# Kernel optimization log

Measured on AMD Instinct MI355X. Metric: run time of the kernel, lower is better.

Reference implementation:

```python
import jax, jax.numpy as jnp
import numpy as np

ALPHA = 1.0
MIN_FEATURE_SIZE = 1.0
SC = 1e-12
EPS_V_FLOOR = 1e-32 ** (1.0 / 6.0)  # ~4.64e-6, floor on gradient magnitude


def setup_inputs() -> dict:
    key = jax.random.key(0)
    eps = jax.random.normal(key, (8192, 8192), dtype=jnp.float32)
    grid_size = jnp.asarray(0.05, dtype=jnp.float32)
    return {"eps": eps, "grid_size": grid_size}


def _ls_derivatives(phi, d):
    # torch.gradient == numpy.gradient with edge_order=1 (central interior, one-sided edges)
    phi_x, phi_y = jnp.gradient(phi, d, d)
    phi_x = phi_x + SC
    phi_y = phi_y + SC
    phi_xx, phi_xy = jnp.gradient(phi_x, d, d)        # second derivs of phi_x
    phi_yy = jnp.gradient(phi_y, d, axis=1)           # only d/dy of phi_y is used
    return phi_x, phi_y, phi_xx, phi_xy, phi_yy


def reference(eps, grid_size):
    ex, ey, exx, exy, eyy = _ls_derivatives(eps, grid_size)
    pi_d = jnp.pi / (1.1 * MIN_FEATURE_SIZE)
    eps_v = jnp.maximum(jnp.sqrt(ex * ex + ey * ey), jnp.float32(EPS_V_FLOOR))
    k = (ex * ex * eyy - 2.0 * ex * ey * exy + ey * ey * exx) / (eps_v ** 3)
    curve_const = jnp.abs(k * jnp.arctan(eps_v / (eps + 1e-6))) - pi_d
    return jnp.nansum(ALPHA * jnp.maximum(curve_const, 0.0) * grid_size ** 2)
```

## Files before the change

kernel.cpp:

```cpp
#include <hip/hip_runtime.h>
#include <math.h>


typedef float f2 __attribute__((ext_vector_type(2)));
typedef float f4 __attribute__((ext_vector_type(4)));

constexpr float SCF = 1e-12f;
constexpr float EVF = 4.6415888336e-6f;
constexpr float PID = 2.8559933214452666f;
constexpr float PIH = 1.5707963268f;
constexpr int   RS  = 64;

struct Row { f4 lo, hi; };

__device__ __forceinline__ float C(const Row& r, int k) {
    return k < 4 ? r.lo[k] : r.hi[k - 4];
}
__device__ __forceinline__ void load_row(Row& r, const float* p) {
    r.lo = *(const f4*)p;
    r.hi = *(const f4*)(p + 4);
}
__device__ __forceinline__ f2 mk(float a, float b) { f2 v; v.x = a; v.y = b; return v; }
__device__ __forceinline__ f2 fma2(f2 a, f2 b, f2 c) { return __builtin_elementwise_fma(a, b, c); }
__device__ __forceinline__ f2 max2(f2 a, f2 b) { return __builtin_elementwise_max(a, b); }
__device__ __forceinline__ f2 min2(f2 a, f2 b) { return __builtin_elementwise_min(a, b); }
__device__ __forceinline__ f2 abs2(f2 a) { return __builtin_elementwise_abs(a); }
__device__ __forceinline__ f2 rcp2(f2 a) {
    return mk(__builtin_amdgcn_rcpf(a.x), __builtin_amdgcn_rcpf(a.y));
}
__device__ __forceinline__ f2 rsq2(f2 a) {
    return mk(__builtin_amdgcn_rsqf(a.x), __builtin_amdgcn_rsqf(a.y));
}

__device__ __forceinline__ f2 compute_pair(const Row& R0, const Row& R1,
                                           const Row& R2, const Row& R3,
                                           const Row& R4, const Row& R5,
                                           f2 c1, f2 c2) {
    f2 dif[6];
    #pragma unroll
    for (int k = 0; k < 6; ++k)
        dif[k] = mk(C(R3, k + 1) - C(R1, k + 1),
                    C(R4, k + 1) - C(R2, k + 1));
    f2 Pz[8];
    #pragma unroll
    for (int k = 0; k < 8; ++k)
        Pz[k] = mk(C(R2, k), C(R3, k));

    f2 part = mk(0.0f, 0.0f);
    #pragma unroll
    for (int q = 0; q < 4; ++q) {
        const f2 c00  = Pz[q + 2];
        const f2 u    = dif[q + 1];
        const f2 v    = Pz[q + 3] - Pz[q + 1];
        const f2 exxr = fma2(mk(-2.0f, -2.0f), c00,
                             mk(C(R4, q + 2) + C(R0, q + 2),
                                C(R5, q + 2) + C(R1, q + 2)));
        const f2 eyyr = fma2(mk(-2.0f, -2.0f), c00, Pz[q + 4] + Pz[q]);
        const f2 exyr = dif[q + 2] - dif[q];

        const f2 uu  = u * u;
        const f2 vv  = v * v;
        const f2 r2  = uu + vv;
        const f2 rsq = rsq2(r2);
        const f2 N   = fma2(uu, eyyr, fma2(-2.0f * (u * v), exyr, vv * exxr));
        const f2 r3  = rsq * rsq * rsq;
        const f2 kabs = abs2(N) * min2(c1 * r3, c2);
        const f2 ev   = max2(c1 * (r2 * rsq), mk(EVF, EVF));

        const f2 aw = abs2(c00 + 1e-6f);
        const f2 mx = max2(ev, aw);
        const f2 mn = min2(ev, aw);
        const f2 t  = mn * rcp2(mx);
        const f2 t2 = t * t;
        f2 pl = fma2(t2, mk(-0.01172120f, -0.01172120f), mk(0.05265332f, 0.05265332f));
        pl = fma2(t2, pl, mk(-0.11643287f, -0.11643287f));
        pl = fma2(t2, pl, mk(0.19354346f, 0.19354346f));
        pl = fma2(t2, pl, mk(-0.33262347f, -0.33262347f));
        pl = fma2(t2, pl, mk(0.99997726f, 0.99997726f));
        pl = pl * t;
        f2 at;
        at.x = (ev.x > aw.x) ? PIH - pl.x : pl.x;
        at.y = (ev.y > aw.y) ? PIH - pl.y : pl.y;

        part = part + max2(fma2(kabs, at, mk(-PID, -PID)), mk(0.0f, 0.0f));
    }
    return part;
}

__device__ __forceinline__ float eg(const float* __restrict__ e, int n, int i, int j) {
    return e[(size_t)i * (size_t)n + j];
}
__device__ __forceinline__ float gex(const float* __restrict__ e, int n, int i, int j,
                                     float inv_d, float inv_2d) {
    float v;
    if (i == 0)          v = (eg(e, n, 1, j) - eg(e, n, 0, j)) * inv_d;
    else if (i == n - 1) v = (eg(e, n, n - 1, j) - eg(e, n, n - 2, j)) * inv_d;
    else                 v = (eg(e, n, i + 1, j) - eg(e, n, i - 1, j)) * inv_2d;
    return v + SCF;
}
__device__ __forceinline__ float gey(const float* __restrict__ e, int n, int i, int j,
                                     float inv_d, float inv_2d) {
    float v;
    if (j == 0)          v = (eg(e, n, i, 1) - eg(e, n, i, 0)) * inv_d;
    else if (j == n - 1) v = (eg(e, n, i, n - 1) - eg(e, n, i, n - 2)) * inv_d;
    else                 v = (eg(e, n, i, j + 1) - eg(e, n, i, j - 1)) * inv_2d;
    return v + SCF;
}

__global__ __launch_bounds__(256, 4)
void fab_fused(const float* __restrict__ eps, const float* __restrict__ gs,
               float* __restrict__ ws, int n, int G2, int nfr) {
    const float d      = *gs;
    const float inv_2d = 0.5f / d;
    const float c1s    = inv_2d;
    const float c2s    = 1e16f * (inv_2d * inv_2d) * (inv_2d * inv_2d);

    float acc = 0.0f;

    const int gg = blockIdx.x * 256 + threadIdx.x;
    const bool valid = gg < G2;
    const int gc = min(gg, G2 - 1);
    const int i0 = 2 + RS * blockIdx.y;
    const int count = min(RS, (n - 2) - i0);
    const float*  pj = eps + 4 * (size_t)gc;
    const size_t  sn = (size_t)n;

    Row s0, s1, s2, s3, s4, s5, s6, s7;
    load_row(s0, pj + (size_t)(i0 - 2) * sn);
    load_row(s1, pj + (size_t)(i0 - 1) * sn);
    load_row(s2, pj + (size_t)(i0    ) * sn);
    load_row(s3, pj + (size_t)(i0 + 1) * sn);
    load_row(s4, pj + (size_t)(i0 + 2) * sn);
    load_row(s5, pj + (size_t)(i0 + 3) * sn);
    const float* pnext = pj + (size_t)(i0 + 4) * sn;

    if (threadIdx.x < 96) {
        const int bflat = blockIdx.y * gridDim.x + blockIdx.x;
        const int idx = bflat * 96 + (int)threadIdx.x;
        if (idx < nfr) {
            const float inv_d = inv_2d + inv_2d;
            int i, j;
            if (idx < 4 * n) {
                const int rr = (idx >= n) + (idx >= 2 * n) + (idx >= 3 * n);
                j = idx - rr * n;
                i = (rr < 2) ? rr : (n - 4) + rr;
            } else {
                const int t = idx - 4 * n;
                i = 2 + (t >> 3);
                const int cc = t & 7;
                j = (cc < 2) ? cc : (n - 8) + cc;
            }

            const float ex0 = gex(eps, n, i, j, inv_d, inv_2d);
            const float ey0 = gey(eps, n, i, j, inv_d, inv_2d);

            float exx, exy, eyy;
            if (i == 0)
                exx = (gex(eps, n, 1, j, inv_d, inv_2d) - ex0) * inv_d;
            else if (i == n - 1)
                exx = (ex0 - gex(eps, n, n - 2, j, inv_d, inv_2d)) * inv_d;
            else
                exx = (gex(eps, n, i + 1, j, inv_d, inv_2d)
                     - gex(eps, n, i - 1, j, inv_d, inv_2d)) * inv_2d;

            if (j == 0)
                exy = (gex(eps, n, i, 1, inv_d, inv_2d) - ex0) * inv_d;
            else if (j == n - 1)
                exy = (ex0 - gex(eps, n, i, n - 2, inv_d, inv_2d)) * inv_d;
            else
                exy = (gex(eps, n, i, j + 1, inv_d, inv_2d)
                     - gex(eps, n, i, j - 1, inv_d, inv_2d)) * inv_2d;

            if (j == 0)
                eyy = (gey(eps, n, i, 1, inv_d, inv_2d) - ey0) * inv_d;
            else if (j == n - 1)
                eyy = (ey0 - gey(eps, n, i, n - 2, inv_d, inv_2d)) * inv_d;
            else
                eyy = (gey(eps, n, i, j + 1, inv_d, inv_2d)
                     - gey(eps, n, i, j - 1, inv_d, inv_2d)) * inv_2d;

            const float ev = fmaxf(__builtin_amdgcn_sqrtf(fmaf(ex0, ex0, ey0 * ey0)), EVF);
            const float num = fmaf(ex0 * ex0, eyy,
                              fmaf(-2.0f * ex0 * ey0, exy, ey0 * ey0 * exx));
            const float kabs = fabsf(num) * __builtin_amdgcn_rcpf(ev * ev * ev);

            const float aw = fabsf(eg(eps, n, i, j) + 1e-6f);
            const float mx = fmaxf(ev, aw);
            const float mn = fminf(ev, aw);
            const float t  = mn * __builtin_amdgcn_rcpf(mx);
            const float t2 = t * t;
            float pl = fmaf(t2, -0.01172120f, 0.05265332f);
            pl = fmaf(t2, pl, -0.11643287f);
            pl = fmaf(t2, pl, 0.19354346f);
            pl = fmaf(t2, pl, -0.33262347f);
            pl = fmaf(t2, pl, 0.99997726f);
            pl *= t;
            const float at = (ev > aw) ? (PIH - pl) : pl;

            acc += fmaxf(fmaf(kabs, at, -PID), 0.0f);
        }
    }

    {
        const f2 c1 = mk(c1s, c1s);
        const f2 c2 = mk(c2s, c2s);

        f2 acc2 = mk(0.0f, 0.0f);
        #define PHASEP(ph, A0, A1, A2, A3, A4, A5, L0, L1)                    \
        {                                                                     \
            const int k = kbase + 2 * (ph);                                   \
            if (k < count) {                                                  \
                if (k + 2 < count) {                                          \
                    load_row(L0, pnext);                                      \
                    load_row(L1, pnext + sn);                                 \
                }                                                             \
                pnext += 2 * sn;                                              \
                acc2 = acc2 + compute_pair(A0, A1, A2, A3, A4, A5, c1, c2);   \
            }                                                                 \
        }

        #pragma unroll 1
        for (int kbase = 0; kbase < RS; kbase += 8) {
            PHASEP(0, s0, s1, s2, s3, s4, s5, s6, s7)
            PHASEP(1, s2, s3, s4, s5, s6, s7, s0, s1)
            PHASEP(2, s4, s5, s6, s7, s0, s1, s2, s3)
            PHASEP(3, s6, s7, s0, s1, s2, s3, s4, s5)
        }
        #undef PHASEP

        if (valid) acc += acc2.x + acc2.y;
    }

    __shared__ float wsum[4];
    #pragma unroll
    for (int off = 32; off; off >>= 1)
        acc += __shfl_down(acc, off, 64);
    if ((threadIdx.x & 63) == 0) wsum[threadIdx.x >> 6] = acc;
    __syncthreads();
    if (threadIdx.x == 0)
        ws[blockIdx.y * gridDim.x + blockIdx.x] =
            wsum[0] + wsum[1] + wsum[2] + wsum[3];
}

__global__ __launch_bounds__(256)
void fab_finish(const float* __restrict__ ws, const float* __restrict__ gs,
                float* __restrict__ out, int nb) {
    __shared__ float wsum[4];
    float v = 0.0f;
    for (int i = threadIdx.x; i < nb; i += 256) v += ws[i];
    #pragma unroll
    for (int off = 32; off; off >>= 1)
        v += __shfl_down(v, off, 64);
    if ((threadIdx.x & 63) == 0) wsum[threadIdx.x >> 6] = v;
    __syncthreads();
    if (threadIdx.x == 0) {
        const float d = *gs;
        out[0] = (wsum[0] + wsum[1] + wsum[2] + wsum[3]) * d * d;
    }
}

extern "C" void kernel_launch(void* const* d_in, const int* in_sizes, int n_in,
                              void* d_out, int out_size, void* d_ws, size_t ws_size,
                              hipStream_t stream) {
    const float* eps = (const float*)d_in[0];
    const float* gs  = (const float*)d_in[1];
    float* out = (float*)d_out;
    float* ws  = (float*)d_ws;

    const long long tot = (long long)in_sizes[0];
    const int n = (int)(sqrt((double)tot) + 0.5);

    const int G2  = (n - 8) / 4;
    const int nstrip = (n - 4 + RS - 1) / RS;
    const int nfr = 4 * n + 8 * (n - 4);

    dim3 block(256, 1);
    dim3 grid(n / 1024, nstrip);
    fab_fused<<<grid, block, 0, stream>>>(eps, gs, ws, n, G2, nfr);
    fab_finish<<<1, 256, 0, stream>>>(ws, gs, out, grid.x * grid.y);
}
```

Before: 90.47 us.

## Vectorize side-column frame handling per row and stagger strip start rows

Side-column frame points are now handled one row per thread. Each thread loads a 5x12 window with float4 reads and computes all 8 edge points from registers, replacing scattered scalar gathers that did one point per thread. This lets only 40 threads per block do frame work instead of 96, which shortens the divergent prologue. The main strip sweep is also rotated by a block-dependent offset of 0, 16, 32 or 48 rows, so neighbouring blocks start at different rows. That staggering spreads DRAM access across channels, but costs an extra halo reload of 6 rows and a second loop for the wrapped portion.

```diff
diff --git a/kernel.cpp b/kernel.cpp
--- a/kernel.cpp
+++ b/kernel.cpp
@@ -10,6 +10,7 @@
 constexpr float PID = 2.8559933214452666f;
 constexpr float PIH = 1.5707963268f;
 constexpr int   RS  = 64;
+constexpr int   FT  = 40;
 
 struct Row { f4 lo, hi; };
 
@@ -87,6 +88,26 @@
     return part;
 }
 
+__device__ __forceinline__ float penalty_scalar(float ex, float ey, float exx,
+                                                float exy, float eyy, float w) {
+    const float ev = fmaxf(__builtin_amdgcn_sqrtf(fmaf(ex, ex, ey * ey)), EVF);
+    const float num = fmaf(ex * ex, eyy, fmaf(-2.0f * ex * ey, exy, ey * ey * exx));
+    const float kabs = fabsf(num) * __builtin_amdgcn_rcpf(ev * ev * ev);
+    const float aw = fabsf(w + 1e-6f);
+    const float mx = fmaxf(ev, aw);
+    const float mn = fminf(ev, aw);
+    const float t  = mn * __builtin_amdgcn_rcpf(mx);
+    const float t2 = t * t;
+    float pl = fmaf(t2, -0.01172120f, 0.05265332f);
+    pl = fmaf(t2, pl, -0.11643287f);
+    pl = fmaf(t2, pl, 0.19354346f);
+    pl = fmaf(t2, pl, -0.33262347f);
+    pl = fmaf(t2, pl, 0.99997726f);
+    pl *= t;
+    const float at = (ev > aw) ? (PIH - pl) : pl;
+    return fmaxf(fmaf(kabs, at, -PID), 0.0f);
+}
+
 __device__ __forceinline__ float eg(const float* __restrict__ e, int n, int i, int j) {
     return e[(size_t)i * (size_t)n + j];
 }
@@ -109,51 +130,26 @@
 
 __global__ __launch_bounds__(256, 4)
 void fab_fused(const float* __restrict__ eps, const float* __restrict__ gs,
-               float* __restrict__ ws, int n, int G2, int nfr) {
+               float* __restrict__ ws, int n, int G2) {
     const float d      = *gs;
     const float inv_2d = 0.5f / d;
+    const float inv_d  = inv_2d + inv_2d;
     const float c1s    = inv_2d;
     const float c2s    = 1e16f * (inv_2d * inv_2d) * (inv_2d * inv_2d);
+    const int bflat    = blockIdx.y * gridDim.x + blockIdx.x;
 
     float acc = 0.0f;
 
-    const int gg = blockIdx.x * 256 + threadIdx.x;
-    const bool valid = gg < G2;
-    const int gc = min(gg, G2 - 1);
-    const int i0 = 2 + RS * blockIdx.y;
-    const int count = min(RS, (n - 2) - i0);
-    const float*  pj = eps + 4 * (size_t)gc;
-    const size_t  sn = (size_t)n;
-
-    Row s0, s1, s2, s3, s4, s5, s6, s7;
-    load_row(s0, pj + (size_t)(i0 - 2) * sn);
-    load_row(s1, pj + (size_t)(i0 - 1) * sn);
-    load_row(s2, pj + (size_t)(i0    ) * sn);
-    load_row(s3, pj + (size_t)(i0 + 1) * sn);
-    load_row(s4, pj + (size_t)(i0 + 2) * sn);
-    load_row(s5, pj + (size_t)(i0 + 3) * sn);
-    const float* pnext = pj + (size_t)(i0 + 4) * sn;
-
-    if (threadIdx.x < 96) {
-        const int bflat = blockIdx.y * gridDim.x + blockIdx.x;
-        const int idx = bflat * 96 + (int)threadIdx.x;
-        if (idx < nfr) {
-            const float inv_d = inv_2d + inv_2d;
-            int i, j;
-            if (idx < 4 * n) {
-                const int rr = (idx >= n) + (idx >= 2 * n) + (idx >= 3 * n);
-                j = idx - rr * n;
-                i = (rr < 2) ? rr : (n - 4) + rr;
-            } else {
-                const int t = idx - 4 * n;
-                i = 2 + (t >> 3);
-                const int cc = t & 7;
-                j = (cc < 2) ? cc : (n - 8) + cc;
-            }
+    if (threadIdx.x < FT) {
+        const int t = bflat * FT + (int)threadIdx.x;
+        const int ntop = 4 * n;
+        if (t < ntop) {
+            const int rr = (t >= n) + (t >= 2 * n) + (t >= 3 * n);
+            const int j = t - rr * n;
+            const int i = (rr < 2) ? rr : (n - 4) + rr;
 
             const float ex0 = gex(eps, n, i, j, inv_d, inv_2d);
             const float ey0 = gey(eps, n, i, j, inv_d, inv_2d);
-
             float exx, exy, eyy;
             if (i == 0)
                 exx = (gex(eps, n, 1, j, inv_d, inv_2d) - ex0) * inv_d;
@@ -162,7 +158,6 @@
             else
                 exx = (gex(eps, n, i + 1, j, inv_d, inv_2d)
                      - gex(eps, n, i - 1, j, inv_d, inv_2d)) * inv_2d;
-
             if (j == 0)
                 exy = (gex(eps, n, i, 1, inv_d, inv_2d) - ex0) * inv_d;
             else if (j == n - 1)
@@ -170,7 +165,6 @@
             else
                 exy = (gex(eps, n, i, j + 1, inv_d, inv_2d)
                      - gex(eps, n, i, j - 1, inv_d, inv_2d)) * inv_2d;
-
             if (j == 0)
                 eyy = (gey(eps, n, i, 1, inv_d, inv_2d) - ey0) * inv_d;
             else if (j == n - 1)
@@ -179,54 +173,100 @@
                 eyy = (gey(eps, n, i, j + 1, inv_d, inv_2d)
                      - gey(eps, n, i, j - 1, inv_d, inv_2d)) * inv_2d;
 
-            const float ev = fmaxf(__builtin_amdgcn_sqrtf(fmaf(ex0, ex0, ey0 * ey0)), EVF);
-            const float num = fmaf(ex0 * ex0, eyy,
-                              fmaf(-2.0f * ex0 * ey0, exy, ey0 * ey0 * exx));
-            const float kabs = fabsf(num) * __builtin_amdgcn_rcpf(ev * ev * ev);
-
-            const float aw = fabsf(eg(eps, n, i, j) + 1e-6f);
-            const float mx = fmaxf(ev, aw);
-            const float mn = fminf(ev, aw);
-            const float t  = mn * __builtin_amdgcn_rcpf(mx);
-            const float t2 = t * t;
-            float pl = fmaf(t2, -0.01172120f, 0.05265332f);
-            pl = fmaf(t2, pl, -0.11643287f);
-            pl = fmaf(t2, pl, 0.19354346f);
-            pl = fmaf(t2, pl, -0.33262347f);
-            pl = fmaf(t2, pl, 0.99997726f);
-            pl *= t;
-            const float at = (ev > aw) ? (PIH - pl) : pl;
-
-            acc += fmaxf(fmaf(kabs, at, -PID), 0.0f);
+            acc += penalty_scalar(ex0, ey0, exx, exy, eyy, eg(eps, n, i, j));
+        } else if (t < ntop + (n - 4)) {
+            const int i = 2 + (t - ntop);
+            float W[5][12];
+            const float* rb = eps + (size_t)(i - 2) * (size_t)n;
+            #pragma unroll
+            for (int r = 0; r < 5; ++r) {
+                const f4 a = *(const f4*)(rb + (size_t)r * n);
+                const f4 b = *(const f4*)(rb + (size_t)r * n + (n - 8));
+                const f4 c = *(const f4*)(rb + (size_t)r * n + (n - 4));
+                #pragma unroll
+                for (int k = 0; k < 4; ++k) {
+                    W[r][k] = a[k]; W[r][4 + k] = b[k]; W[r][8 + k] = c[k];
+                }
+            }
+            auto exW = [&](int r, int wc) {
+                return (W[r + 1][wc] - W[r - 1][wc]) * inv_2d + SCF;
+            };
+            auto eyW = [&](int wc) {
+                if (wc == 0)  return (W[2][1] - W[2][0]) * inv_d + SCF;
+                if (wc == 11) return (W[2][11] - W[2][10]) * inv_d + SCF;
+                return (W[2][wc + 1] - W[2][wc - 1]) * inv_2d + SCF;
+            };
+            #pragma unroll
+            for (int m = 0; m < 8; ++m) {
+                const int wc = (m < 2) ? m : m + 4;
+                const float ex0 = exW(2, wc);
+                const float ey0 = eyW(wc);
+                const float exx = (exW(3, wc) - exW(1, wc)) * inv_2d;
+                float exy, eyy;
+                if (wc == 0) {
+                    exy = (exW(2, 1) - exW(2, 0)) * inv_d;
+                    eyy = (eyW(1) - eyW(0)) * inv_d;
+                } else if (wc == 11) {
+                    exy = (exW(2, 11) - exW(2, 10)) * inv_d;
+                    eyy = (eyW(11) - eyW(10)) * inv_d;
+                } else {
+                    exy = (exW(2, wc + 1) - exW(2, wc - 1)) * inv_2d;
+                    eyy = (eyW(wc + 1) - eyW(wc - 1)) * inv_2d;
+                }
+                acc += penalty_scalar(ex0, ey0, exx, exy, eyy, W[2][wc]);
+            }
         }
     }
 
     {
+        const int gg = blockIdx.x * 256 + threadIdx.x;
+        const bool valid = gg < G2;
+        const int gc = min(gg, G2 - 1);
+        const int i0 = 2 + RS * blockIdx.y;
+        const int count = min(RS, (n - 2) - i0);
+        const float* pj = eps + 4 * (size_t)gc;
+        const size_t sn = (size_t)n;
         const f2 c1 = mk(c1s, c1s);
         const f2 c2 = mk(c2s, c2s);
 
         f2 acc2 = mk(0.0f, 0.0f);
-        #define PHASEP(ph, A0, A1, A2, A3, A4, A5, L0, L1)                    \
-        {                                                                     \
-            const int k = kbase + 2 * (ph);                                   \
-            if (k < count) {                                                  \
-                if (k + 2 < count) {                                          \
-                    load_row(L0, pnext);                                      \
-                    load_row(L1, pnext + sn);                                 \
+
+        auto sweep = [&](int start, int len) {
+            Row s0, s1, s2, s3, s4, s5, s6, s7;
+            load_row(s0, pj + (size_t)(start - 2) * sn);
+            load_row(s1, pj + (size_t)(start - 1) * sn);
+            load_row(s2, pj + (size_t)(start    ) * sn);
+            load_row(s3, pj + (size_t)(start + 1) * sn);
+            load_row(s4, pj + (size_t)(start + 2) * sn);
+            load_row(s5, pj + (size_t)(start + 3) * sn);
+            const float* pnext = pj + (size_t)(start + 4) * sn;
+
+            #define PHASEP(ph, A0, A1, A2, A3, A4, A5, L0, L1)                \
+            {                                                                 \
+                const int k = kbase + 2 * (ph);                               \
+                if (k < len) {                                                \
+                    if (k + 2 < len) {                                        \
+                        load_row(L0, pnext);                                  \
+                        load_row(L1, pnext + sn);                             \
+                    }                                                         \
+                    pnext += 2 * sn;                                          \
+                    acc2 = acc2 + compute_pair(A0, A1, A2, A3, A4, A5,        \
+                                               c1, c2);                       \
                 }                                                             \
-                pnext += 2 * sn;                                              \
-                acc2 = acc2 + compute_pair(A0, A1, A2, A3, A4, A5, c1, c2);   \
-            }                                                                 \
-        }
-
-        #pragma unroll 1
-        for (int kbase = 0; kbase < RS; kbase += 8) {
-            PHASEP(0, s0, s1, s2, s3, s4, s5, s6, s7)
-            PHASEP(1, s2, s3, s4, s5, s6, s7, s0, s1)
-            PHASEP(2, s4, s5, s6, s7, s0, s1, s2, s3)
-            PHASEP(3, s6, s7, s0, s1, s2, s3, s4, s5)
-        }
-        #undef PHASEP
+            }
+            #pragma unroll 1
+            for (int kbase = 0; kbase < len; kbase += 8) {
+                PHASEP(0, s0, s1, s2, s3, s4, s5, s6, s7)
+                PHASEP(1, s2, s3, s4, s5, s6, s7, s0, s1)
+                PHASEP(2, s4, s5, s6, s7, s0, s1, s2, s3)
+                PHASEP(3, s6, s7, s0, s1, s2, s3, s4, s5)
+            }
+            #undef PHASEP
+        };
+
+        const int off = 16 * (bflat & 3);
+        sweep(i0 + off, count - off);
+        if (off > 0) sweep(i0, off);
 
         if (valid) acc += acc2.x + acc2.y;
     }
@@ -238,8 +278,7 @@
     if ((threadIdx.x & 63) == 0) wsum[threadIdx.x >> 6] = acc;
     __syncthreads();
     if (threadIdx.x == 0)
-        ws[blockIdx.y * gridDim.x + blockIdx.x] =
-            wsum[0] + wsum[1] + wsum[2] + wsum[3];
+        ws[bflat] = wsum[0] + wsum[1] + wsum[2] + wsum[3];
 }
 
 __global__ __launch_bounds__(256)
@@ -270,12 +309,11 @@
     const long long tot = (long long)in_sizes[0];
     const int n = (int)(sqrt((double)tot) + 0.5);
 
-    const int G2  = (n - 8) / 4;
+    const int G2 = (n - 8) / 4;
     const int nstrip = (n - 4 + RS - 1) / RS;
-    const int nfr = 4 * n + 8 * (n - 4);
 
     dim3 block(256, 1);
     dim3 grid(n / 1024, nstrip);
-    fab_fused<<<grid, block, 0, stream>>>(eps, gs, ws, n, G2, nfr);
+    fab_fused<<<grid, block, 0, stream>>>(eps, gs, ws, n, G2);
     fab_finish<<<1, 256, 0, stream>>>(ws, gs, out, grid.x * grid.y);
 }
```

Result: faster. 85.29 us (-5.7%).
